# Kernel tuning notes

Hardware: AMD Instinct MI355X
Metric: run time of the kernel (lower is better)

The kernel has to match this reference:

```python
import jax, jax.numpy as jnp
import numpy as np
import math

D_MODEL = 1024
N_HEADS = 16
HEAD_DIM = D_MODEL // N_HEADS
TOP_FACTOR = 5
B, L = 2, 2048


def setup_inputs() -> dict:
    key = jax.random.key(0)
    ks = jax.random.split(key, 12)
    f = lambda k, shp: jax.random.normal(k, shp, dtype=jnp.float32)
    w = lambda k: f(k, (D_MODEL, D_MODEL)) * 0.02
    return {
        "queries": f(ks[0], (B, L, D_MODEL)),
        "keys": f(ks[1], (B, L, D_MODEL)),
        "values": f(ks[2], (B, L, D_MODEL)),
        "Wq": w(ks[3]), "bq": jnp.zeros((D_MODEL,), jnp.float32),
        "Wk": w(ks[4]), "bk": jnp.zeros((D_MODEL,), jnp.float32),
        "Wv": w(ks[5]), "bv": jnp.zeros((D_MODEL,), jnp.float32),
        "Wo": w(ks[6]), "bo": jnp.zeros((D_MODEL,), jnp.float32),
    }


def reference(queries, keys, values, Wq, bq, Wk, bk, Wv, bv, Wo, bo):
    Bq, L_q, _ = queries.shape
    L_k = keys.shape[1]
    H, D = N_HEADS, HEAD_DIM

    def proj(x, W, b, Lx):
        return (x @ W.T + b).reshape(Bq, Lx, H, D).transpose(0, 2, 1, 3)  # (B,H,L,D)

    q = proj(queries, Wq, bq, L_q)
    k = proj(keys, Wk, bk, L_k)
    v = proj(values, Wv, bv, L_k)

    # Normalized QK score pass for query ranking
    q_norm = q / jnp.linalg.norm(q, axis=-1, keepdims=True)
    k_norm = k / jnp.linalg.norm(k, axis=-1, keepdims=True)
    scores_all = jnp.einsum("bhqd,bhkd->bhqk", q_norm, k_norm)  # (B,H,Lq,Lk)
    mean_scores = scores_all.mean(axis=-1)                        # (B,H,Lq)

    u = max(1, L_q // TOP_FACTOR)
    _, top_idx = jax.lax.top_k(mean_scores, u)                    # (B,H,u)

    # Gather selected queries and run dense attention on them
    q_sel = jnp.take_along_axis(q, top_idx[..., None], axis=2)    # (B,H,u,D)
    scores = jnp.einsum("bhud,bhkd->bhuk", q_sel, k) / math.sqrt(D)
    attn = jax.nn.softmax(scores, axis=-1)
    ctx_sel = jnp.einsum("bhuk,bhkd->bhud", attn, v)              # (B,H,u,D)

    # Scatter back into zero context tensor
    bidx = jnp.arange(Bq)[:, None, None]
    hidx = jnp.arange(H)[None, :, None]
    context = jnp.zeros((Bq, H, L_q, D), dtype=queries.dtype)
    context = context.at[bidx, hidx, top_idx].set(ctx_sel)

    out = context.transpose(0, 2, 1, 3).reshape(Bq, L_q, H * D)
    return out @ Wo.T + bo
```

## Files before the change

### kernel.cpp

```cpp
#include <hip/hip_runtime.h>
#include <math.h>

#define NB 2
#define NL 2048
#define NH 16
#define ND 64
#define NDM 1024
#define NU 409
#define NUP 416
#define NBH (NB*NH)
#define NROWS (NB*NL)
#define NRTOT (NB*NH*NL)
#define MTOT (NBH*NUP)

typedef short bf16x8 __attribute__((ext_vector_type(8)));
typedef short bf16x4 __attribute__((ext_vector_type(4)));
typedef float f32x4  __attribute__((ext_vector_type(4)));

__device__ __forceinline__ short f2bf(float x) {
  unsigned u = __float_as_uint(x);
  return (short)((u + 0x7FFFu + ((u >> 16) & 1u)) >> 16);
}
__device__ __forceinline__ float bf2f(short s) {
  return __uint_as_float(((unsigned)(unsigned short)s) << 16);
}

__device__ __forceinline__ void gload16(const short* g, short* l) {
  __builtin_amdgcn_global_load_lds(
      (const __attribute__((address_space(1))) void*)g,
      (__attribute__((address_space(3))) void*)l, 16, 0, 0);
}

struct SplitDesc { const float* in; short* a; short* b; short* c; int nc; int nblk; };
struct SplitArgs { SplitDesc d[7]; };

__global__ __launch_bounds__(256) void msplit_k(SplitArgs args) {
  const SplitDesc d = args.d[blockIdx.z];
  if ((int)blockIdx.x >= d.nblk) return;
  const size_t i = (size_t)blockIdx.x * 256 + threadIdx.x;
  const float4 x0 = ((const float4*)d.in)[2*i];
  const float4 x1 = ((const float4*)d.in)[2*i + 1];
  float x[8] = {x0.x,x0.y,x0.z,x0.w, x1.x,x1.y,x1.z,x1.w};
  bf16x8 va, vb;
  #pragma unroll
  for (int j = 0; j < 8; ++j) {
    const short A = f2bf(x[j]);
    va[j] = A;
    vb[j] = f2bf(x[j] - bf2f(A));
  }
  *(bf16x8*)(d.a + 8*i) = va;
  if (d.nc >= 2) *(bf16x8*)(d.b + 8*i) = vb;
}

struct GemmDesc {
  const short* X[2];
  const short* W[2];
  const float* bias;
  short* KbfVt;
  double* kpart;
  float* sq;
  int sbeg, send;
  int mode;
};
struct GemmArgs { GemmDesc d[3]; };

__global__ __launch_bounds__(256, 3) void gemm_mega_k(GemmArgs args) {
  __shared__ short As[128*64];
  __shared__ short Bs[128*64];
  const int fid = blockIdx.x;
  const int xcd = fid & 7, jd = fid >> 3;
  const int s = jd % 3, jj = jd / 3;
  const int tile = (xcd << 5) + jj;
  const int bx = tile & 7, by = tile >> 3;
  const GemmDesc d = args.d[s];
  const int tid = threadIdx.x;
  const int wv = tid >> 6, L = tid & 63;
  const int lr = L & 15, lg = L >> 4;
  const int n0 = bx << 7, m0 = by << 7;
  const int wm = (wv >> 1) << 6, wn = (wv & 1) << 6;
  const int sr = tid >> 3, ssl = tid & 7;

  f32x4 acc[4][4];
  #pragma unroll
  for (int i = 0; i < 4; ++i)
    #pragma unroll
    for (int j = 0; j < 4; ++j) acc[i][j] = (f32x4){0.f,0.f,0.f,0.f};

  for (int step = d.sbeg; step < d.send; ++step) {
    const int c = step >> 4, kk = (step & 15) << 6;
    const short *Xg, *Wg;
    switch (c) {
      case 0:  Xg = d.X[0]; Wg = d.W[0]; break;
      case 1:  Xg = d.X[0]; Wg = d.W[1]; break;
      default: Xg = d.X[1]; Wg = d.W[0]; break;
    }
    #pragma unroll
    for (int j = 0; j < 4; ++j) {
      const int row = (j << 5) + sr;
      const int slot = (ssl ^ (row & 7)) << 3;
      gload16(Xg + (size_t)(m0 + row) * NDM + kk + slot, As + (j << 11) + (tid << 3));
      gload16(Wg + (size_t)(n0 + row) * NDM + kk + slot, Bs + (j << 11) + (tid << 3));
    }
    __syncthreads();
    #pragma unroll
    for (int c2 = 0; c2 < 2; ++c2) {
      const int sl = (((c2 << 2) + lg) ^ (lr & 7)) << 3;
      bf16x8 af[4], bfr[4];
      #pragma unroll
      for (int t = 0; t < 4; ++t) {
        af[t]  = *(const bf16x8*)(As + ((wm + (t << 4) + lr) << 6) + sl);
        bfr[t] = *(const bf16x8*)(Bs + ((wn + (t << 4) + lr) << 6) + sl);
      }
      #pragma unroll
      for (int mt = 0; mt < 4; ++mt)
        #pragma unroll
        for (int nt = 0; nt < 4; ++nt)
          acc[mt][nt] = __builtin_amdgcn_mfma_f32_16x16x32_bf16(bfr[nt], af[mt], acc[mt][nt], 0, 0, 0);
    }
    __syncthreads();
  }

  if (d.mode == 1) {
    const int b2 = by >> 4;
    const int hw = (bx << 1) + (wv & 1);
    const int bh = (b2 << 4) + hw;
    const int seg = ((by & 15) << 1) + (wv >> 1);
    float kv[4][4][4];
    double inv[4];
    #pragma unroll
    for (int mt = 0; mt < 4; ++mt) {
      float ss = 0.f;
      #pragma unroll
      for (int nt = 0; nt < 4; ++nt) {
        const int n = n0 + wn + (nt << 4) + (lg << 2);
        const float4 b4 = *(const float4*)(d.bias + n);
        kv[mt][nt][0] = acc[mt][nt][0] + b4.x;
        kv[mt][nt][1] = acc[mt][nt][1] + b4.y;
        kv[mt][nt][2] = acc[mt][nt][2] + b4.z;
        kv[mt][nt][3] = acc[mt][nt][3] + b4.w;
        #pragma unroll
        for (int j = 0; j < 4; ++j) ss += kv[mt][nt][j] * kv[mt][nt][j];
      }
      ss += __shfl_xor(ss, 16);
      ss += __shfl_xor(ss, 32);
      inv[mt] = 1.0 / sqrt((double)ss);
    }
    #pragma unroll
    for (int mt = 0; mt < 4; ++mt) {
      const int l = (m0 + wm + (mt << 4) + lr) & (NL - 1);
      short* kp = d.KbfVt + (((size_t)bh * NL + l) << 6);
      #pragma unroll
      for (int nt = 0; nt < 4; ++nt) {
        const int dd = (nt << 4) + (lg << 2);
        bf16x4 o;
        #pragma unroll
        for (int j = 0; j < 4; ++j) o[j] = f2bf(kv[mt][nt][j]);
        *(bf16x4*)(kp + dd) = o;
      }
    }
    #pragma unroll
    for (int nt = 0; nt < 4; ++nt) {
      double p[4];
      #pragma unroll
      for (int j = 0; j < 4; ++j) {
        p[j] = 0.0;
        #pragma unroll
        for (int mt = 0; mt < 4; ++mt) p[j] += (double)kv[mt][nt][j] * inv[mt];
        p[j] += __shfl_xor(p[j], 1);
        p[j] += __shfl_xor(p[j], 2);
        p[j] += __shfl_xor(p[j], 4);
        p[j] += __shfl_xor(p[j], 8);
      }
      if (lr == 0) {
        const int dd = (nt << 4) + (lg << 2);
        double* kp = d.kpart + ((((size_t)bh << 5) + seg) << 6) + dd;
        kp[0] = p[0]; kp[1] = p[1]; kp[2] = p[2]; kp[3] = p[3];
      }
    }
  } else if (d.mode == 3) {
    const int b2 = by >> 4;
    const int hw = (bx << 1) + (wv & 1);
    const int bh = (b2 << 4) + hw;
    #pragma unroll
    for (int mt = 0; mt < 4; ++mt) {
      float kv[4][4];
      float ss = 0.f;
      #pragma unroll
      for (int nt = 0; nt < 4; ++nt) {
        const int n = n0 + wn + (nt << 4) + (lg << 2);
        const float4 b4 = *(const float4*)(d.bias + n);
        kv[nt][0] = acc[mt][nt][0] + b4.x;
        kv[nt][1] = acc[mt][nt][1] + b4.y;
        kv[nt][2] = acc[mt][nt][2] + b4.z;
        kv[nt][3] = acc[mt][nt][3] + b4.w;
        #pragma unroll
        for (int j = 0; j < 4; ++j) ss += kv[nt][j] * kv[nt][j];
      }
      ss += __shfl_xor(ss, 16);
      ss += __shfl_xor(ss, 32);
      const int l = (m0 + wm + (mt << 4) + lr) & (NL - 1);
      if (lg == 0) d.sq[((size_t)bh << 11) + l] = ss;
      short* qp = d.KbfVt + (((size_t)bh * NL + l) << 6);
      #pragma unroll
      for (int nt = 0; nt < 4; ++nt) {
        const int dd = (nt << 4) + (lg << 2);
        bf16x4 o;
        #pragma unroll
        for (int j = 0; j < 4; ++j) o[j] = f2bf(kv[nt][j]);
        *(bf16x4*)(qp + dd) = o;
      }
    }
  } else {
    #pragma unroll
    for (int nt = 0; nt < 4; ++nt) {
      const int nl = wn + (nt << 4) + (lg << 2);
      const float4 b4 = *(const float4*)(d.bias + n0 + nl);
      #pragma unroll
      for (int j2 = 0; j2 < 4; ++j2) {
        const int row = nl + j2;
        short* Tp = (row & 64) ? Bs : As;
        const int rr = row & 63;
        const float bj = (j2 == 0) ? b4.x : (j2 == 1) ? b4.y : (j2 == 2) ? b4.z : b4.w;
        const int sw = (row & 7) << 3;
        #pragma unroll
        for (int mt = 0; mt < 4; ++mt) {
          const int m = wm + (mt << 4) + lr;
          Tp[rr * 128 + (m ^ sw)] = f2bf(acc[mt][nt][j2] + bj);
        }
      }
    }
    __syncthreads();
    {
      const int r = tid >> 1, seg2 = tid & 1;
      const short* Tp = (r & 64) ? Bs : As;
      const int rr = r & 63, sw = (r & 7) << 3;
      const int ngl = n0 + r, h = ngl >> 6, dd2 = ngl & 63;
      const int bb = m0 >> 11, ll = m0 & (NL - 1);
      short* dst = d.KbfVt + (((size_t)((((bb << 4) + h) << 6) + dd2)) << 11) + ll + (seg2 << 6);
      #pragma unroll
      for (int i = 0; i < 8; ++i)
        *(bf16x8*)(dst + (i << 3)) =
            *(const bf16x8*)(Tp + rr * 128 + (((seg2 << 6) + (i << 3)) ^ sw));
    }
  }
}

__global__ __launch_bounds__(256) void wtilde_k(const float* __restrict__ Wq,
                                                const float* __restrict__ bq,
                                                const double* __restrict__ kpart,
                                                float* __restrict__ wt,
                                                double* __restrict__ s0) {
  __shared__ double kb[64];
  const int bh = blockIdx.x, h = bh & 15;
  const int tid = threadIdx.x;
  if (tid < 64) {
    double s = 0.0;
    #pragma unroll
    for (int seg = 0; seg < 32; ++seg)
      s += kpart[((((size_t)bh << 5) + seg) << 6) + tid];
    kb[tid] = s * (1.0 / NL);
  }
  __syncthreads();
  const int j = (blockIdx.y << 8) + tid;
  double a = 0.0;
  #pragma unroll 8
  for (int d = 0; d < 64; ++d)
    a += (double)Wq[(((size_t)((h << 6) + d)) << 10) + j] * kb[d];
  wt[((size_t)bh << 10) + j] = (float)a;
  if (blockIdx.y == 0 && tid < 64) {
    double p = (double)bq[(h << 6) + tid] * kb[tid];
    #pragma unroll
    for (int off = 32; off > 0; off >>= 1) p += __shfl_xor(p, off);
    if (tid == 0) s0[bh] = p;
  }
}

__global__ __launch_bounds__(256) void dotqms_k(const float* __restrict__ x,
                                                const float* __restrict__ sqv,
                                                const float* __restrict__ wt,
                                                const double* __restrict__ s0,
                                                float* __restrict__ ms) {
  __shared__ float xs[1024];
  __shared__ double sm[16][16];
  const int r = blockIdx.x, b = r >> 11, l = r & (NL - 1);
  const int tid = threadIdx.x;
  ((float4*)xs)[tid] = ((const float4*)(x + ((size_t)r << 10)))[tid];
  __syncthreads();
  const int h = tid >> 4, t = tid & 15;
  const float* w = wt + ((size_t)((b << 4) + h) << 10);
  double a = 0.0;
  #pragma unroll 8
  for (int i = 0; i < 64; ++i) {
    const int j = t + (i << 4);
    a += (double)xs[j] * (double)w[j];
  }
  sm[h][t] = a;
  __syncthreads();
  if (tid < 16) {
    double s = 0.0;
    #pragma unroll
    for (int t2 = 0; t2 < 16; ++t2) s += sm[tid][t2];
    const size_t ro = (((size_t)(b << 4) + tid) << 11) + l;
    ms[ro] = (float)((s + s0[(b << 4) + tid]) / sqrt((double)sqv[ro]));
  }
}

__global__ __launch_bounds__(256) void select_rank_k(const float* __restrict__ ms,
                                                     int* __restrict__ sel,
                                                     int* __restrict__ invsel) {
  __shared__ unsigned long long keys[NL];
  const int bh = blockIdx.x >> 3, seg = blockIdx.x & 7;
  const int tid = threadIdx.x;
  for (int l = tid; l < NL; l += 256) {
    unsigned u = __float_as_uint(ms[(size_t)bh * NL + l]);
    u = (u & 0x80000000u) ? ~u : (u | 0x80000000u);
    keys[l] = ((unsigned long long)u << 32) | (unsigned)(NL - 1 - l);
  }
  __syncthreads();
  const int r = (seg << 8) + tid;
  const unsigned long long mine = keys[r];
  int cnt = 0;
  #pragma unroll 8
  for (int l = 0; l < NL; ++l) cnt += (keys[l] > mine) ? 1 : 0;
  if (cnt < NU) sel[bh*NU + cnt] = r;
  invsel[(size_t)bh * NL + r] = (cnt < NU) ? cnt : NU;
}

__global__ __launch_bounds__(512) void fattn_k(const short* __restrict__ Qbf,
                                               const int* __restrict__ sel,
                                               const short* __restrict__ Kbf,
                                               const short* __restrict__ Vt,
                                               short* __restrict__ Csel) {
  __shared__ short S[32*2048];
  __shared__ float inv_s[32];
  int bid = blockIdx.x;
  bid = (bid & 7) * 52 + (bid >> 3);
  const int m0 = bid << 5;
  const int bh = m0 / NUP;
  const int u0 = m0 - bh * NUP;
  const int tid = threadIdx.x;
  const int w = tid >> 6, L = tid & 63;
  const int lr = L & 15, lg = L >> 4;

  bf16x8 qf[2][2];
  #pragma unroll
  for (int mt = 0; mt < 2; ++mt) {
    const int u = u0 + mt*16 + lr;
    const int lq = (u < NU) ? sel[bh*NU + u] : 0;
    const short* qp = Qbf + (((size_t)bh*NL + lq) << 6) + lg*8;
    qf[mt][0] = *(const bf16x8*)qp;
    qf[mt][1] = *(const bf16x8*)(qp + 32);
  }
  const int nb = w << 8;
  const short* kb0 = Kbf + (((size_t)bh*NL + nb + lr) << 6) + lg*8;
  #pragma unroll 2
  for (int nt = 0; nt < 16; ++nt) {
    const short* kp = kb0 + ((size_t)nt << 10);
    const bf16x8 kf0 = *(const bf16x8*)kp;
    const bf16x8 kf1 = *(const bf16x8*)(kp + 32);
    #pragma unroll
    for (int mt = 0; mt < 2; ++mt) {
      f32x4 a = {0.f,0.f,0.f,0.f};
      a = __builtin_amdgcn_mfma_f32_16x16x32_bf16(kf0, qf[mt][0], a, 0, 0, 0);
      a = __builtin_amdgcn_mfma_f32_16x16x32_bf16(kf1, qf[mt][1], a, 0, 0, 0);
      const int m = mt*16 + lr;
      bf16x4 o;
      #pragma unroll
      for (int r = 0; r < 4; ++r) o[r] = f2bf(a[r] * 0.125f);
      const int byteoff = (m << 12) + ((((nb + nt*16 + lg*4) << 1)) ^ ((m & 7) << 4));
      *(bf16x4*)((char*)S + byteoff) = o;
    }
  }
  __syncthreads();

  #pragma unroll
  for (int j = 0; j < 4; ++j) {
    const int R = (w << 2) + j;
    char* rowp = (char*)S + (R << 12);
    const int sw = (R & 7) << 4;
    bf16x8 v[4];
    #pragma unroll
    for (int i = 0; i < 4; ++i)
      v[i] = *(const bf16x8*)(rowp + (((L << 6) + (i << 4)) ^ sw));
    float f[32];
    #pragma unroll
    for (int i = 0; i < 4; ++i)
      #pragma unroll
      for (int e = 0; e < 8; ++e) f[i*8+e] = bf2f(v[i][e]);
    float mx = f[0];
    #pragma unroll
    for (int i = 1; i < 32; ++i) mx = fmaxf(mx, f[i]);
    #pragma unroll
    for (int off = 32; off > 0; off >>= 1) mx = fmaxf(mx, __shfl_xor(mx, off));
    float sum = 0.f;
    #pragma unroll
    for (int i = 0; i < 32; ++i) { f[i] = __expf(f[i] - mx); sum += f[i]; }
    #pragma unroll
    for (int off = 32; off > 0; off >>= 1) sum += __shfl_xor(sum, off);
    bf16x8 p[4];
    #pragma unroll
    for (int i = 0; i < 4; ++i)
      #pragma unroll
      for (int e = 0; e < 8; ++e) p[i][e] = f2bf(f[i*8+e]);
    #pragma unroll
    for (int i = 0; i < 4; ++i)
      *(bf16x8*)(rowp + (((L << 6) + (i << 4)) ^ sw)) = p[i];
    if (L == 0) inv_s[R] = 1.f / sum;
  }
  __syncthreads();

  {
    const int mt = w & 1, dt = w >> 1;
    const int m = mt*16 + lr;
    const char* arow = (const char*)S + (m << 12);
    const int sw = (m & 7) << 4;
    const short* vrow = Vt + (((size_t)bh*ND + dt*16 + lr) << 11) + lg*8;
    f32x4 acc0 = {0.f,0.f,0.f,0.f}, acc1 = {0.f,0.f,0.f,0.f};
    for (int k0 = 0; k0 < NL; k0 += 64) {
      const bf16x8 p0 = *(const bf16x8*)(arow + ((((k0 + lg*8) << 1)) ^ sw));
      const bf16x8 p1 = *(const bf16x8*)(arow + ((((k0 + 32 + lg*8) << 1)) ^ sw));
      const bf16x8 v0 = *(const bf16x8*)(vrow + k0);
      const bf16x8 v1 = *(const bf16x8*)(vrow + k0 + 32);
      acc0 = __builtin_amdgcn_mfma_f32_16x16x32_bf16(p0, v0, acc0, 0, 0, 0);
      acc1 = __builtin_amdgcn_mfma_f32_16x16x32_bf16(p1, v1, acc1, 0, 0, 0);
    }
    const int ub = u0 + mt*16 + (lg << 2);
    #pragma unroll
    for (int r = 0; r < 4; ++r) {
      float val = (acc0[r] + acc1[r]) * inv_s[mt*16 + (lg << 2) + r];
      if (ub + r >= NU) val = 0.f;
      const size_t off = (((size_t)m0 + mt*16 + (lg << 2) + r) << 6) + dt*16 + lr;
      Csel[off] = f2bf(val);
    }
  }
}

struct OselArgs {
  const short* X;
  const short* Wa; const short* Wb;
  float* C0; float* C1; float* C2; float* C3;
  const int* invsel;
};

__global__ __launch_bounds__(256, 3) void gemm_osel_k(OselArgs ar) {
  __shared__ short As[128*64];
  __shared__ short Bs[128*64];
  __shared__ int utbl[2048];
  const int fid = blockIdx.x;
  const int xcd = fid & 7, jd = fid >> 3;
  const int zi = jd & 3;
  const int o = (xcd << 5) + (jd >> 2);
  const int bx = o & 7, by = o >> 3;
  const int sbeg = zi << 3, send = sbeg + 8;
  float* C = (zi == 0) ? ar.C0 : (zi == 1) ? ar.C1 : (zi == 2) ? ar.C2 : ar.C3;
  const int tid = threadIdx.x;
  const int wv = tid >> 6, L = tid & 63;
  const int lr = L & 15, lg = L >> 4;
  const int n0 = bx << 7, m0 = by << 7;
  const int wm = (wv >> 1) << 6, wn = (wv & 1) << 6;
  const int sr = tid >> 3, ssl = tid & 7;
  const int b2 = by >> 4;

  #pragma unroll
  for (int e = 0; e < 8; ++e) {
    const int idx = (tid << 3) + e;
    const int row = idx >> 4, h = idx & 15;
    utbl[idx] = ar.invsel[((((size_t)b2 << 4) + h) << 11) + ((m0 + row) & (NL - 1))];
  }
  __syncthreads();

  f32x4 acc[4][4];
  #pragma unroll
  for (int i = 0; i < 4; ++i)
    #pragma unroll
    for (int j = 0; j < 4; ++j) acc[i][j] = (f32x4){0.f,0.f,0.f,0.f};

  for (int step = sbeg; step < send; ++step) {
    const int c = step >> 4, kk = (step & 15) << 6;
    const short* Wg = c ? ar.Wb : ar.Wa;
    #pragma unroll
    for (int j = 0; j < 4; ++j) {
      const int row = (j << 5) + sr;
      const int slot = (ssl ^ (row & 7)) << 3;
      const int h = step & 15;
      const int u = utbl[(row << 4) + h];
      gload16(ar.X + (((size_t)((b2 << 4) + h) * NUP + u) << 6) + slot,
              As + (j << 11) + (tid << 3));
      gload16(Wg + (size_t)(n0 + row) * NDM + kk + slot, Bs + (j << 11) + (tid << 3));
    }
    __syncthreads();
    #pragma unroll
    for (int c2 = 0; c2 < 2; ++c2) {
      const int sl = (((c2 << 2) + lg) ^ (lr & 7)) << 3;
      bf16x8 af[4], bfr[4];
      #pragma unroll
      for (int t = 0; t < 4; ++t) {
        af[t]  = *(const bf16x8*)(As + ((wm + (t << 4) + lr) << 6) + sl);
        bfr[t] = *(const bf16x8*)(Bs + ((wn + (t << 4) + lr) << 6) + sl);
      }
      #pragma unroll
      for (int mt = 0; mt < 4; ++mt)
        #pragma unroll
        for (int nt = 0; nt < 4; ++nt)
          acc[mt][nt] = __builtin_amdgcn_mfma_f32_16x16x32_bf16(bfr[nt], af[mt], acc[mt][nt], 0, 0, 0);
    }
    __syncthreads();
  }

  #pragma unroll
  for (int nt = 0; nt < 4; ++nt) {
    const int n = n0 + wn + (nt << 4) + (lg << 2);
    #pragma unroll
    for (int mt = 0; mt < 4; ++mt) {
      const int m = m0 + wm + (mt << 4) + lr;
      *(f32x4*)(C + ((size_t)m << 10) + n) = acc[mt][nt];
    }
  }
}

__global__ __launch_bounds__(256) void oadd_k(float* __restrict__ out,
                                              const float* __restrict__ P1,
                                              const float* __restrict__ P2,
                                              const float* __restrict__ P3,
                                              const float* __restrict__ bo) {
  const size_t i4 = (size_t)blockIdx.x * 256 + threadIdx.x;
  const size_t i = i4 << 2;
  float4 a = *(float4*)(out + i);
  const float4 b = *(const float4*)(P1 + i);
  const float4 c = *(const float4*)(P2 + i);
  const float4 e = *(const float4*)(P3 + i);
  const float4 d = *(const float4*)(bo + ((i4 & 255) << 2));
  a.x += b.x + c.x + e.x + d.x; a.y += b.y + c.y + e.y + d.y;
  a.z += b.z + c.z + e.z + d.z; a.w += b.w + c.w + e.w + d.w;
  *(float4*)(out + i) = a;
}

extern "C" void kernel_launch(void* const* d_in, const int* in_sizes, int n_in,
                              void* d_out, int out_size, void* d_ws, size_t ws_size,
                              hipStream_t stream)
{
  (void)in_sizes; (void)n_in; (void)out_size; (void)ws_size;
  const float* queries = (const float*)d_in[0];
  const float* keys    = (const float*)d_in[1];
  const float* values  = (const float*)d_in[2];
  const float* Wq = (const float*)d_in[3];  const float* bq = (const float*)d_in[4];
  const float* Wk = (const float*)d_in[5];  const float* bk = (const float*)d_in[6];
  const float* Wv = (const float*)d_in[7];  const float* bv = (const float*)d_in[8];
  const float* Wo = (const float*)d_in[9];  const float* bo = (const float*)d_in[10];
  float* out = (float*)d_out;

  char* base = (char*)d_ws;
  #define MB(x) ((size_t)(x) << 20)

  short* Qa   = (short*)(base + MB(0));
  short* Qb2  = (short*)(base + MB(8));
  short* Ka   = (short*)(base + MB(16));
  short* Kb2  = (short*)(base + MB(24));
  short* Kbf  = (short*)(base + MB(32));
  short* Vbf  = (short*)(base + MB(40));
  short* Qbf  = (short*)(base + MB(48));
  float* P1o  = (float*)(base + MB(56));
  short* Vt   = (short*)(base + MB(72));
  short* Wqa  = (short*)(base + MB(80));
  short* Wqb  = (short*)(base + MB(82));
  short* Wka  = (short*)(base + MB(84));
  short* Wkb  = (short*)(base + MB(86));
  short* Wvbf = (short*)(base + MB(88));
  short* Woa  = (short*)(base + MB(90));
  short* Wob  = (short*)(base + MB(92));
  char* sm = base + MB(94);
  double* kpart  = (double*)sm;  sm += 524288;
  float*  wt     = (float*)sm;   sm += 131072;
  double* s0     = (double*)sm;  sm += 512;
  float*  sqv    = (float*)sm;   sm += 262144;
  float*  msb    = (float*)sm;   sm += 262144;
  int*    sel    = (int*)sm;     sm += 65536;
  int*    invsel = (int*)sm;     sm += 262144;

  short* Csel = Vbf;
  float* P2o  = (float*)Ka;
  float* P3o  = (float*)Qa;

  {
    SplitArgs a;
    a.d[0] = {queries, Qa, Qb2, nullptr, 2, 2048};
    a.d[1] = {keys,    Ka, Kb2, nullptr, 2, 2048};
    a.d[2] = {values,  Vbf, nullptr, nullptr, 1, 2048};
    a.d[3] = {Wq, Wqa, Wqb, nullptr, 2, 512};
    a.d[4] = {Wk, Wka, Wkb, nullptr, 2, 512};
    a.d[5] = {Wv, Wvbf, nullptr, nullptr, 1, 512};
    a.d[6] = {Wo, Woa, Wob, nullptr, 2, 512};
    msplit_k<<<dim3(2048,1,7), 256, 0, stream>>>(a);
  }
  {
    GemmArgs g;
    g.d[0] = {{Qa,Qb2},  {Wqa,Wqb},   bq, Qbf, nullptr, sqv,     0, 48, 3};
    g.d[1] = {{Ka,Kb2},  {Wka,Wkb},   bk, Kbf, kpart,   nullptr, 0, 48, 1};
    g.d[2] = {{Vbf,Vbf}, {Wvbf,Wvbf}, bv, Vt,  nullptr, nullptr, 0, 16, 2};
    gemm_mega_k<<<768, 256, 0, stream>>>(g);
  }
  wtilde_k<<<dim3(NBH,4), 256, 0, stream>>>(Wq, bq, kpart, wt, s0);
  dotqms_k<<<NROWS, 256, 0, stream>>>(queries, sqv, wt, s0, msb);
  select_rank_k<<<NBH*8, 256, 0, stream>>>(msb, sel, invsel);

  fattn_k<<<MTOT/32, 512, 0, stream>>>(Qbf, sel, Kbf, Vt, Csel);

  {
    OselArgs oa = {Csel, Woa, Wob, out, P1o, P2o, P3o, invsel};
    gemm_osel_k<<<1024, 256, 0, stream>>>(oa);
  }
  oadd_k<<<4096, 256, 0, stream>>>(out, P1o, P2o, P3o, bo);
}
```

Baseline: 233.9 us.

## Drop split-K in output GEMM, fuse bias epilogue, raise MFMA wave priority

The output projection GEMM no longer splits K four ways into partial buffers followed by a separate reduction kernel. Each block now covers a 64x128 tile over the full K range and adds the bias directly in its epilogue, which removes the oadd kernel and about 48MB of fp32 partial traffic. This halves the grid from 1024 to 512 blocks and makes each block's K loop four times longer. The attention kernel also wraps its MFMA loops in s_setprio to favour matrix-issuing waves.

```diff
diff --git a/kernel.cpp b/kernel.cpp
--- a/kernel.cpp
+++ b/kernel.cpp
@@ -353,6 +353,7 @@
   }
   const int nb = w << 8;
   const short* kb0 = Kbf + (((size_t)bh*NL + nb + lr) << 6) + lg*8;
+  __builtin_amdgcn_s_setprio(1);
   #pragma unroll 2
   for (int nt = 0; nt < 16; ++nt) {
     const short* kp = kb0 + ((size_t)nt << 10);
@@ -371,6 +372,7 @@
       *(bf16x4*)((char*)S + byteoff) = o;
     }
   }
+  __builtin_amdgcn_s_setprio(0);
   __syncthreads();
 
   #pragma unroll
@@ -416,6 +418,7 @@
     const int sw = (m & 7) << 4;
     const short* vrow = Vt + (((size_t)bh*ND + dt*16 + lr) << 11) + lg*8;
     f32x4 acc0 = {0.f,0.f,0.f,0.f}, acc1 = {0.f,0.f,0.f,0.f};
+    __builtin_amdgcn_s_setprio(1);
     for (int k0 = 0; k0 < NL; k0 += 64) {
       const bf16x8 p0 = *(const bf16x8*)(arow + ((((k0 + lg*8) << 1)) ^ sw));
       const bf16x8 p1 = *(const bf16x8*)(arow + ((((k0 + 32 + lg*8) << 1)) ^ sw));
@@ -424,6 +427,7 @@
       acc0 = __builtin_amdgcn_mfma_f32_16x16x32_bf16(p0, v0, acc0, 0, 0, 0);
       acc1 = __builtin_amdgcn_mfma_f32_16x16x32_bf16(p1, v1, acc1, 0, 0, 0);
     }
+    __builtin_amdgcn_s_setprio(0);
     const int ub = u0 + mt*16 + (lg << 2);
     #pragma unroll
     for (int r = 0; r < 4; ++r) {
@@ -438,68 +442,72 @@
 struct OselArgs {
   const short* X;
   const short* Wa; const short* Wb;
-  float* C0; float* C1; float* C2; float* C3;
+  const float* bias;
+  float* C;
   const int* invsel;
 };
 
 __global__ __launch_bounds__(256, 3) void gemm_osel_k(OselArgs ar) {
-  __shared__ short As[128*64];
+  __shared__ short As[64*64];
   __shared__ short Bs[128*64];
-  __shared__ int utbl[2048];
+  __shared__ int utbl[1024];
   const int fid = blockIdx.x;
-  const int xcd = fid & 7, jd = fid >> 3;
-  const int zi = jd & 3;
-  const int o = (xcd << 5) + (jd >> 2);
+  const int xcd = fid & 7, jj = fid >> 3;
+  const int o = (xcd << 6) + jj;
   const int bx = o & 7, by = o >> 3;
-  const int sbeg = zi << 3, send = sbeg + 8;
-  float* C = (zi == 0) ? ar.C0 : (zi == 1) ? ar.C1 : (zi == 2) ? ar.C2 : ar.C3;
   const int tid = threadIdx.x;
   const int wv = tid >> 6, L = tid & 63;
   const int lr = L & 15, lg = L >> 4;
-  const int n0 = bx << 7, m0 = by << 7;
-  const int wm = (wv >> 1) << 6, wn = (wv & 1) << 6;
+  const int n0 = bx << 7, m0 = by << 6;
+  const int wm = (wv >> 1) << 5, wn = (wv & 1) << 6;
   const int sr = tid >> 3, ssl = tid & 7;
-  const int b2 = by >> 4;
+  const int b2 = by >> 5;
 
   #pragma unroll
-  for (int e = 0; e < 8; ++e) {
-    const int idx = (tid << 3) + e;
+  for (int e = 0; e < 4; ++e) {
+    const int idx = (tid << 2) + e;
     const int row = idx >> 4, h = idx & 15;
     utbl[idx] = ar.invsel[((((size_t)b2 << 4) + h) << 11) + ((m0 + row) & (NL - 1))];
   }
   __syncthreads();
 
-  f32x4 acc[4][4];
+  f32x4 acc[2][4];
   #pragma unroll
-  for (int i = 0; i < 4; ++i)
+  for (int i = 0; i < 2; ++i)
     #pragma unroll
     for (int j = 0; j < 4; ++j) acc[i][j] = (f32x4){0.f,0.f,0.f,0.f};
 
-  for (int step = sbeg; step < send; ++step) {
+  for (int step = 0; step < 32; ++step) {
     const int c = step >> 4, kk = (step & 15) << 6;
     const short* Wg = c ? ar.Wb : ar.Wa;
     #pragma unroll
-    for (int j = 0; j < 4; ++j) {
+    for (int j = 0; j < 2; ++j) {
       const int row = (j << 5) + sr;
       const int slot = (ssl ^ (row & 7)) << 3;
       const int h = step & 15;
       const int u = utbl[(row << 4) + h];
       gload16(ar.X + (((size_t)((b2 << 4) + h) * NUP + u) << 6) + slot,
               As + (j << 11) + (tid << 3));
+    }
+    #pragma unroll
+    for (int j = 0; j < 4; ++j) {
+      const int row = (j << 5) + sr;
+      const int slot = (ssl ^ (row & 7)) << 3;
       gload16(Wg + (size_t)(n0 + row) * NDM + kk + slot, Bs + (j << 11) + (tid << 3));
     }
     __syncthreads();
     #pragma unroll
     for (int c2 = 0; c2 < 2; ++c2) {
       const int sl = (((c2 << 2) + lg) ^ (lr & 7)) << 3;
-      bf16x8 af[4], bfr[4];
-      #pragma unroll
-      for (int t = 0; t < 4; ++t) {
-        af[t]  = *(const bf16x8*)(As + ((wm + (t << 4) + lr) << 6) + sl);
+      bf16x8 af[2], bfr[4];
+      #pragma unroll
+      for (int t = 0; t < 2; ++t)
+        af[t] = *(const bf16x8*)(As + ((wm + (t << 4) + lr) << 6) + sl);
+      #pragma unroll
+      for (int t = 0; t < 4; ++t)
         bfr[t] = *(const bf16x8*)(Bs + ((wn + (t << 4) + lr) << 6) + sl);
-      }
-      #pragma unroll
-      for (int mt = 0; mt < 4; ++mt)
+      #pragma unroll
+      for (int mt = 0; mt < 2; ++mt)
         #pragma unroll
         for (int nt = 0; nt < 4; ++nt)
           acc[mt][nt] = __builtin_amdgcn_mfma_f32_16x16x32_bf16(bfr[nt], af[mt], acc[mt][nt], 0, 0, 0);
@@ -510,29 +518,15 @@
   #pragma unroll
   for (int nt = 0; nt < 4; ++nt) {
     const int n = n0 + wn + (nt << 4) + (lg << 2);
-    #pragma unroll
-    for (int mt = 0; mt < 4; ++mt) {
+    const float4 b4 = *(const float4*)(ar.bias + n);
+    #pragma unroll
+    for (int mt = 0; mt < 2; ++mt) {
+      f32x4 a = acc[mt][nt];
+      a[0] += b4.x; a[1] += b4.y; a[2] += b4.z; a[3] += b4.w;
       const int m = m0 + wm + (mt << 4) + lr;
-      *(f32x4*)(C + ((size_t)m << 10) + n) = acc[mt][nt];
-    }
-  }
-}
-
-__global__ __launch_bounds__(256) void oadd_k(float* __restrict__ out,
-                                              const float* __restrict__ P1,
-                                              const float* __restrict__ P2,
-                                              const float* __restrict__ P3,
-                                              const float* __restrict__ bo) {
-  const size_t i4 = (size_t)blockIdx.x * 256 + threadIdx.x;
-  const size_t i = i4 << 2;
-  float4 a = *(float4*)(out + i);
-  const float4 b = *(const float4*)(P1 + i);
-  const float4 c = *(const float4*)(P2 + i);
-  const float4 e = *(const float4*)(P3 + i);
-  const float4 d = *(const float4*)(bo + ((i4 & 255) << 2));
-  a.x += b.x + c.x + e.x + d.x; a.y += b.y + c.y + e.y + d.y;
-  a.z += b.z + c.z + e.z + d.z; a.w += b.w + c.w + e.w + d.w;
-  *(float4*)(out + i) = a;
+      *(f32x4*)(ar.C + ((size_t)m << 10) + n) = a;
+    }
+  }
 }
 
 extern "C" void kernel_launch(void* const* d_in, const int* in_sizes, int n_in,
@@ -559,16 +553,15 @@
   short* Kbf  = (short*)(base + MB(32));
   short* Vbf  = (short*)(base + MB(40));
   short* Qbf  = (short*)(base + MB(48));
-  float* P1o  = (float*)(base + MB(56));
-  short* Vt   = (short*)(base + MB(72));
-  short* Wqa  = (short*)(base + MB(80));
-  short* Wqb  = (short*)(base + MB(82));
-  short* Wka  = (short*)(base + MB(84));
-  short* Wkb  = (short*)(base + MB(86));
-  short* Wvbf = (short*)(base + MB(88));
-  short* Woa  = (short*)(base + MB(90));
-  short* Wob  = (short*)(base + MB(92));
-  char* sm = base + MB(94);
+  short* Vt   = (short*)(base + MB(56));
+  short* Wqa  = (short*)(base + MB(64));
+  short* Wqb  = (short*)(base + MB(66));
+  short* Wka  = (short*)(base + MB(68));
+  short* Wkb  = (short*)(base + MB(70));
+  short* Wvbf = (short*)(base + MB(72));
+  short* Woa  = (short*)(base + MB(74));
+  short* Wob  = (short*)(base + MB(76));
+  char* sm = base + MB(78);
   double* kpart  = (double*)sm;  sm += 524288;
   float*  wt     = (float*)sm;   sm += 131072;
   double* s0     = (double*)sm;  sm += 512;
@@ -578,8 +571,6 @@
   int*    invsel = (int*)sm;     sm += 262144;
 
   short* Csel = Vbf;
-  float* P2o  = (float*)Ka;
-  float* P3o  = (float*)Qa;
 
   {
     SplitArgs a;
@@ -606,8 +597,7 @@
   fattn_k<<<MTOT/32, 512, 0, stream>>>(Qbf, sel, Kbf, Vt, Csel);
 
   {
-    OselArgs oa = {Csel, Woa, Wob, out, P1o, P2o, P3o, invsel};
-    gemm_osel_k<<<1024, 256, 0, stream>>>(oa);
-  }
-  oadd_k<<<4096, 256, 0, stream>>>(out, P1o, P2o, P3o, bo);
-}
+    OselArgs oa = {Csel, Woa, Wob, bo, out, invsel};
+    gemm_osel_k<<<512, 256, 0, stream>>>(oa);
+  }
+}
```

Result: faster. 224.5 us (-4.0%).
